# Kernel tuning notes

Measured on AMD Instinct MI355X. Metric: run time of the kernel, lower is better.

## Reference

```python
import jax, jax.numpy as jnp
import numpy as np

D_MODEL = 1024
ED = 2048          # d_inner = 2 * d_model
N = 16             # d_state
DT_RANK = 64
K = 4              # d_conv
BETA = 0.6
ALPHA = 1.0
B_SZ, L = 1, 2048


def setup_inputs() -> dict:
    key = jax.random.key(0)
    ks = jax.random.split(key, 9)
    s = 0.02
    x = jax.random.normal(ks[0], (B_SZ, L, D_MODEL), jnp.float32)
    W_in = jax.random.normal(ks[1], (2 * ED, D_MODEL), jnp.float32) * s
    conv_w = jax.random.normal(ks[2], (ED, K), jnp.float32) * s
    conv_b = jax.random.normal(ks[3], (ED,), jnp.float32) * s
    W_x = jax.random.normal(ks[4], (DT_RANK + 2 * N, ED), jnp.float32) * s
    dt_std = DT_RANK ** -0.5
    W_dt = jax.random.uniform(ks[5], (ED, DT_RANK), jnp.float32, -dt_std, dt_std)
    # dt bias init: inverse-softplus of dt in [dt_min, dt_max]
    dt = jnp.exp(jax.random.uniform(ks[6], (ED,), jnp.float32)
                 * (np.log(0.1) - np.log(0.001)) + np.log(0.001))
    dt = jnp.clip(dt, 1e-4)
    b_dt = dt + jnp.log(-jnp.expm1(-dt))
    A_log = jnp.log(jnp.tile(jnp.arange(1, N + 1, dtype=jnp.float32), (ED, 1)))
    D = jnp.ones((ED,), jnp.float32)
    W_out = jax.random.normal(ks[7], (D_MODEL, ED), jnp.float32) * s
    return {"x": x, "W_in": W_in, "conv_w": conv_w, "conv_b": conv_b,
            "W_x": W_x, "W_dt": W_dt, "b_dt": b_dt, "A_log": A_log,
            "D": D, "W_out": W_out}


def _depthwise_causal_conv(xc, conv_w, conv_b):
    # xc: (B, L, ED); torch Conv1d(groups=ED, padding=K-1)[..., :L] == causal conv
    lhs = jnp.transpose(xc, (0, 2, 1))                       # (B, ED, L)
    lhs = jnp.pad(lhs, ((0, 0), (0, 0), (K - 1, 0)))
    out = jax.lax.conv_general_dilated(lhs, conv_w[:, None, :], (1,), 'VALID',
                                       feature_group_count=ED)  # (B, ED, L)
    return jnp.transpose(out, (0, 2, 1)) + conv_b


def _ssm_momentum(xc, W_x, W_dt, b_dt, A_log, D):
    A = -jnp.exp(A_log)                                      # (ED, N)
    dBC = xc @ W_x.T                                         # (B, L, dt_rank + 2N)
    delta, Bm, Cm = jnp.split(dBC, [DT_RANK, DT_RANK + N], axis=-1)
    delta = jax.nn.softplus(delta @ W_dt.T + b_dt)           # (B, L, ED)
    deltaA = jnp.exp(delta[..., None] * A)                   # (B, L, ED, N)
    u = ALPHA * delta[..., None] * Bm[:, :, None, :] * xc[..., None]  # (B, L, ED, N)

    def step(carry, inp):
        h, v = carry
        dA_t, u_t = inp
        v = BETA * v + u_t
        h = dA_t * h + v
        return (h, v), h

    h0 = jnp.zeros((xc.shape[0], ED, N), xc.dtype)
    _, hs = jax.lax.scan(step, (h0, h0),
                         (jnp.moveaxis(deltaA, 1, 0), jnp.moveaxis(u, 1, 0)))
    y = jnp.einsum('lben,bln->ble', hs, Cm)                  # (B, L, ED)
    return y + D * xc


def reference(x, W_in, conv_w, conv_b, W_x, W_dt, b_dt, A_log, D, W_out):
    xz = x @ W_in.T                                          # (B, L, 2*ED)
    xc, z = jnp.split(xz, 2, axis=-1)
    xc = jax.nn.silu(_depthwise_causal_conv(xc, conv_w, conv_b))
    y = _ssm_momentum(xc, W_x, W_dt, b_dt, A_log, D)
    return (y * jax.nn.silu(z)) @ W_out.T                    # (B, L, d_model)
```

## Files before the change

kernel.cpp:

```cpp
#include <hip/hip_runtime.h>
#include <hip/hip_bf16.h>
#include <math.h>

#define L 2048
#define DM 1024
#define ED 2048
#define NST 16
#define DTR 64
#define BETA 0.6f
#define NCHUNK 64
#define LCH 32
#define SPLITS 16
#define SPLIT4 4

typedef __bf16 bf16_t;
typedef __bf16 bf16x8 __attribute__((ext_vector_type(8)));
typedef __bf16 bf16x4 __attribute__((ext_vector_type(4)));
typedef float  floatx4 __attribute__((ext_vector_type(4)));


__global__ void k_fill(float* __restrict__ p, float v, int n) {
    int i = blockIdx.x * 256 + threadIdx.x;
    if (i < n) p[i] = v;
}

__global__ void k_cvt_all(const float4* __restrict__ s0, bf16x4* __restrict__ d0,
                          const float4* __restrict__ s1, bf16x4* __restrict__ d1,
                          const float4* __restrict__ s2, bf16x4* __restrict__ d2,
                          const float4* __restrict__ s3, bf16x4* __restrict__ d3,
                          const float4* __restrict__ s4, bf16x4* __restrict__ d4) {
    int i = blockIdx.x * 256 + threadIdx.x;
    const float4* s; bf16x4* d; int j;
    if (i < 524288)        { s = s0; d = d0; j = i; }
    else if (i < 1572864)  { s = s1; d = d1; j = i - 524288; }
    else if (i < 1622016)  { s = s2; d = d2; j = i - 1572864; }
    else if (i < 1654784)  { s = s3; d = d3; j = i - 1622016; }
    else                   { s = s4; d = d4; j = i - 1654784; }
    float4 f = s[j];
    bf16x4 o;
    o[0] = (bf16_t)f.x; o[1] = (bf16_t)f.y; o[2] = (bf16_t)f.z; o[3] = (bf16_t)f.w;
    d[j] = o;
}

template<int EPI, bool GUARD>
__global__ __launch_bounds__(256)
void k_gemm_bt(const bf16_t* __restrict__ X, const bf16_t* __restrict__ W,
               float* __restrict__ C, int M, int N, int K, int ldc, int ksz,
               const float* __restrict__ bias) {
    __shared__ bf16_t As[128 * 32];
    __shared__ bf16_t Bs[128 * 32];
    const int tid  = threadIdx.x;
    const int bx   = blockIdx.x, by = blockIdx.y;
    const int kbase = blockIdx.z * ksz;
    const size_t zoff = (size_t)blockIdx.z * M * ldc;
    const int wave = tid >> 6, lane = tid & 63;
    const int wm   = (wave >> 1) * 64;
    const int wn   = (wave & 1) * 64;
    const int quad = lane >> 4, l16 = lane & 15;

    floatx4 acc[4][4];
#pragma unroll
    for (int i = 0; i < 4; i++)
#pragma unroll
        for (int j = 0; j < 4; j++)
            acc[i][j] = (floatx4){0.f, 0.f, 0.f, 0.f};

    for (int kt = kbase; kt < kbase + ksz; kt += 32) {
        if (GUARD) {
#pragma unroll
            for (int p = 0; p < 2; p++) {
                int e = p * 2048 + tid * 8;
                int r = e >> 5, c = e & 31;
                int arow = by * 128 + r;
                *(float4*)(&As[r * 32 + c]) =
                    *(const float4*)(&X[(size_t)arow * K + kt + c]);
                int brow = bx * 128 + r;
                float4 bv = make_float4(0.f, 0.f, 0.f, 0.f);
                if (brow < N) bv = *(const float4*)(&W[(size_t)brow * K + kt + c]);
                *(float4*)(&Bs[r * 32 + c]) = bv;
            }
        } else {
#pragma unroll
            for (int p = 0; p < 2; p++) {
                int e = p * 2048 + tid * 8;
                int r = e >> 5, c = e & 31;
                __builtin_amdgcn_global_load_lds(
                    (const __attribute__((address_space(1))) void*)&X[(size_t)(by * 128 + r) * K + kt + c],
                    (__attribute__((address_space(3))) void*)&As[e], 16, 0, 0);
                __builtin_amdgcn_global_load_lds(
                    (const __attribute__((address_space(1))) void*)&W[(size_t)(bx * 128 + r) * K + kt + c],
                    (__attribute__((address_space(3))) void*)&Bs[e], 16, 0, 0);
            }
        }
        __syncthreads();

        bf16x8 af[4], bfr[4];
#pragma unroll
        for (int mt = 0; mt < 4; mt++)
            af[mt] = *(const bf16x8*)(&As[(wm + mt * 16 + l16) * 32 + quad * 8]);
#pragma unroll
        for (int nt = 0; nt < 4; nt++)
            bfr[nt] = *(const bf16x8*)(&Bs[(wn + nt * 16 + l16) * 32 + quad * 8]);
#pragma unroll
        for (int mt = 0; mt < 4; mt++)
#pragma unroll
            for (int nt = 0; nt < 4; nt++)
                acc[mt][nt] = __builtin_amdgcn_mfma_f32_16x16x32_bf16(
                    af[mt], bfr[nt], acc[mt][nt], 0, 0, 0);
        __syncthreads();
    }

#pragma unroll
    for (int mt = 0; mt < 4; mt++) {
#pragma unroll
        for (int nt = 0; nt < 4; nt++) {
            int col = bx * 128 + wn + nt * 16 + l16;
            if (!GUARD || col < N) {
#pragma unroll
                for (int r4 = 0; r4 < 4; r4++) {
                    int row = by * 128 + wm + mt * 16 + quad * 4 + r4;
                    float v = acc[mt][nt][r4];
                    size_t off = zoff + (size_t)row * ldc + col;
                    if (EPI == 0) {
                        C[off] = v;
                    } else if (EPI == 1) {
                        v += bias[col];
                        v = (v > 20.f) ? v : __logf(1.f + __expf(v));
                        ((bf16_t*)C)[off] = (bf16_t)v;
                    } else {
                        ((bf16_t*)C)[off] = (bf16_t)v;
                    }
                }
            }
        }
    }
}

__global__ void k_red4(const bf16x8* __restrict__ part, float4* __restrict__ out) {
    int i = blockIdx.x * 256 + threadIdx.x;
    const int stride = L * DM / 8;
    bf16x8 a = part[i], b = part[i + stride];
    bf16x8 c = part[i + 2 * stride], d = part[i + 3 * stride];
    float4 o0, o1;
    o0.x = (float)a[0] + (float)b[0] + (float)c[0] + (float)d[0];
    o0.y = (float)a[1] + (float)b[1] + (float)c[1] + (float)d[1];
    o0.z = (float)a[2] + (float)b[2] + (float)c[2] + (float)d[2];
    o0.w = (float)a[3] + (float)b[3] + (float)c[3] + (float)d[3];
    o1.x = (float)a[4] + (float)b[4] + (float)c[4] + (float)d[4];
    o1.y = (float)a[5] + (float)b[5] + (float)c[5] + (float)d[5];
    o1.z = (float)a[6] + (float)b[6] + (float)c[6] + (float)d[6];
    o1.w = (float)a[7] + (float)b[7] + (float)c[7] + (float)d[7];
    out[2 * i]     = o0;
    out[2 * i + 1] = o1;
}

__global__ void k_conv_silu(const bf16_t* __restrict__ xz,
                            const float* __restrict__ conv_w,
                            const float* __restrict__ conv_b,
                            bf16_t* __restrict__ xc_bf) {
    int idx = blockIdx.x * 256 + threadIdx.x;
    int e = idx & (ED - 1);
    int t = idx >> 11;
    float w0 = conv_w[e * 4 + 0], w1 = conv_w[e * 4 + 1];
    float w2 = conv_w[e * 4 + 2], w3 = conv_w[e * 4 + 3];
    const bf16_t* col = xz + e;
    float acc = conv_b[e];
    if (t >= 3) acc += w0 * (float)col[(size_t)(t - 3) * 4096];
    if (t >= 2) acc += w1 * (float)col[(size_t)(t - 2) * 4096];
    if (t >= 1) acc += w2 * (float)col[(size_t)(t - 1) * 4096];
    acc += w3 * (float)col[(size_t)t * 4096];
    float s = acc / (1.f + __expf(-acc));
    xc_bf[idx] = (bf16_t)s;
}

__global__ void k_red2(const float* __restrict__ part, float* __restrict__ dBC,
                       bf16_t* __restrict__ dly) {
    int idx = blockIdx.x * 256 + threadIdx.x;
    int t = idx / 96, c = idx - t * 96;
    float s = 0.f;
#pragma unroll
    for (int sp = 0; sp < SPLITS; sp++) s += part[(size_t)sp * L * 96 + idx];
    dBC[idx] = s;
    if (c < 64) dly[t * 64 + c] = (bf16_t)s;
}


__global__ __launch_bounds__(256)
void k_scan_p1(const bf16_t* __restrict__ delta, const bf16_t* __restrict__ xc,
               const float* __restrict__ dBC, const float* __restrict__ A_log,
               float4* __restrict__ summ) {
    const int chunk = blockIdx.x >> 3;
    const int e = (blockIdx.x & 7) * 256 + threadIdx.x;
    float A[NST];
#pragma unroll
    for (int n = 0; n < NST; n++) A[n] = -__expf(A_log[e * NST + n]);
    float h[NST], v[NST], p[NST], q[NST];
#pragma unroll
    for (int n = 0; n < NST; n++) { h[n] = 0.f; v[n] = 0.f; p[n] = 1.f; q[n] = 0.f; }
    float bp = 1.f;
    const int t0 = chunk * LCH;
    for (int i = 0; i < LCH; i++) {
        int t = t0 + i;
        float d   = (float)delta[(size_t)t * ED + e];
        float xcv = (float)xc[(size_t)t * ED + e];
        float du  = d * xcv;
        bp *= BETA;
        const float* Bp = &dBC[t * 96 + 64];
#pragma unroll
        for (int n = 0; n < NST; n++) {
            float a = __expf(d * A[n]);
            v[n] = BETA * v[n] + du * Bp[n];
            h[n] = a * h[n] + v[n];
            p[n] *= a;
            q[n] = a * q[n] + bp;
        }
    }
#pragma unroll
    for (int n = 0; n < NST; n++)
        summ[((size_t)n * NCHUNK + chunk) * ED + e] = make_float4(h[n], v[n], p[n], q[n]);
}

__global__ void k_combine(const float4* __restrict__ summ, float2* __restrict__ inc) {
    int tid = blockIdx.x * 256 + threadIdx.x;
    int n = tid >> 11, e = tid & (ED - 1);
    float h = 0.f, v = 0.f;
    const float bl = 7.9586611e-8f;
#pragma unroll 4
    for (int c = 0; c < NCHUNK; c++) {
        size_t idx = ((size_t)n * NCHUNK + c) * ED + e;
        float4 f = summ[idx];
        inc[idx] = make_float2(h, v);
        float hn = f.z * h + f.w * v + f.x;
        v = bl * v + f.y;
        h = hn;
    }
}

__global__ __launch_bounds__(256)
void k_scan_p2(const bf16_t* __restrict__ delta, const bf16_t* __restrict__ xc,
               const float* __restrict__ dBC, const float* __restrict__ A_log,
               const float2* __restrict__ inc, const float* __restrict__ Dvec,
               const bf16_t* __restrict__ xz, bf16_t* __restrict__ g) {
    const int chunk = blockIdx.x >> 3;
    const int e = (blockIdx.x & 7) * 256 + threadIdx.x;
    float A[NST];
#pragma unroll
    for (int n = 0; n < NST; n++) A[n] = -__expf(A_log[e * NST + n]);
    float h[NST], v[NST];
#pragma unroll
    for (int n = 0; n < NST; n++) {
        float2 s = inc[((size_t)n * NCHUNK + chunk) * ED + e];
        h[n] = s.x; v[n] = s.y;
    }
    const float De = Dvec[e];
    const int t0 = chunk * LCH;
    for (int i = 0; i < LCH; i++) {
        int t = t0 + i;
        float d   = (float)delta[(size_t)t * ED + e];
        float xcv = (float)xc[(size_t)t * ED + e];
        float du  = d * xcv;
        const float* Bp = &dBC[t * 96 + 64];
        const float* Cp = &dBC[t * 96 + 80];
        float yacc = 0.f;
#pragma unroll
        for (int n = 0; n < NST; n++) {
            float a = __expf(d * A[n]);
            v[n] = BETA * v[n] + du * Bp[n];
            h[n] = a * h[n] + v[n];
            yacc += Cp[n] * h[n];
        }
        float z = (float)xz[(size_t)t * 4096 + ED + e];
        float sz = z / (1.f + __expf(-z));
        g[(size_t)t * ED + e] = (bf16_t)((yacc + De * xcv) * sz);
    }
}


extern "C" void kernel_launch(void* const* d_in, const int* in_sizes, int n_in,
                              void* d_out, int out_size, void* d_ws, size_t ws_size,
                              hipStream_t stream) {
    const float* x      = (const float*)d_in[0];
    const float* W_in   = (const float*)d_in[1];
    const float* conv_w = (const float*)d_in[2];
    const float* conv_b = (const float*)d_in[3];
    const float* W_x    = (const float*)d_in[4];
    const float* W_dt   = (const float*)d_in[5];
    const float* b_dt   = (const float*)d_in[6];
    const float* A_log  = (const float*)d_in[7];
    const float* Dv     = (const float*)d_in[8];
    const float* W_out  = (const float*)d_in[9];
    float* out = (float*)d_out;

    constexpr size_t OFF_XZ    = 0;
    constexpr size_t OFF_XC    = 33554432;
    constexpr size_t OFF_C     = 50331648;
    constexpr size_t OFF_DELTA = 58720256;
    constexpr size_t OFF_R1    = 75497472;
    constexpr size_t OFF_XBF   = 109051904;
    constexpr size_t OFF_DBC   = 113246208;
    constexpr size_t OFF_DLY   = 114032640;
    constexpr size_t OFF_WX    = 114294784;
    constexpr size_t OFF_WDT   = 114688000;
    constexpr size_t OFF_WOUT  = 114950144;
    constexpr size_t WS_NEED   = 119144448;

    if (ws_size < WS_NEED) {
        k_fill<<<(out_size + 255) / 256, 256, 0, stream>>>(out, 1.0e9f, out_size);
        return;
    }

    char* ws = (char*)d_ws;
    bf16_t* xz_bf = (bf16_t*)(ws + OFF_XZ);
    bf16_t* part4 = (bf16_t*)(ws + OFF_XZ);
    float2* inc   = (float2*)(ws + OFF_XC);
    bf16_t* xc_bf = (bf16_t*)(ws + OFF_C);
    bf16_t* delta_bf = (bf16_t*)(ws + OFF_DELTA);
    bf16_t* g_bf  = (bf16_t*)(ws + OFF_DELTA + 8388608);
    bf16_t* Win_bf  = (bf16_t*)(ws + OFF_R1);
    float*  part2   = (float*)(ws + OFF_R1 + 16777216);
    float4* summ    = (float4*)(ws + OFF_R1);
    bf16_t* x_bf  = (bf16_t*)(ws + OFF_XBF);
    float*  dBC   = (float*)(ws + OFF_DBC);
    bf16_t* dly   = (bf16_t*)(ws + OFF_DLY);
    bf16_t* Wx_bf  = (bf16_t*)(ws + OFF_WX);
    bf16_t* Wdt_bf = (bf16_t*)(ws + OFF_WDT);
    bf16_t* Wout_bf = (bf16_t*)(ws + OFF_WOUT);

    k_cvt_all<<<8512, 256, 0, stream>>>(
        (const float4*)x,     (bf16x4*)x_bf,
        (const float4*)W_in,  (bf16x4*)Win_bf,
        (const float4*)W_x,   (bf16x4*)Wx_bf,
        (const float4*)W_dt,  (bf16x4*)Wdt_bf,
        (const float4*)W_out, (bf16x4*)Wout_bf);

    {
        dim3 g(4096 / 128, L / 128, 1);
        k_gemm_bt<2, false><<<g, 256, 0, stream>>>(x_bf, Win_bf, (float*)xz_bf, L, 4096, DM, 4096, DM, nullptr);
    }
    k_conv_silu<<<L * ED / 256, 256, 0, stream>>>(xz_bf, conv_w, conv_b, xc_bf);
    {
        dim3 g(1, L / 128, SPLITS);
        k_gemm_bt<0, true><<<g, 256, 0, stream>>>(xc_bf, Wx_bf, part2, L, 96, ED, 96, ED / SPLITS, nullptr);
    }
    k_red2<<<L * 96 / 256, 256, 0, stream>>>(part2, dBC, dly);
    {
        dim3 g(ED / 128, L / 128, 1);
        k_gemm_bt<1, false><<<g, 256, 0, stream>>>(dly, Wdt_bf, (float*)delta_bf, L, ED, DTR, ED, DTR, b_dt);
    }
    k_scan_p1<<<NCHUNK * 8, 256, 0, stream>>>(delta_bf, xc_bf, dBC, A_log, summ);
    k_combine<<<ED * NST / 256, 256, 0, stream>>>(summ, inc);
    k_scan_p2<<<NCHUNK * 8, 256, 0, stream>>>(delta_bf, xc_bf, dBC, A_log, inc, Dv, xz_bf, g_bf);
    {
        dim3 g(DM / 128, L / 128, SPLIT4);
        k_gemm_bt<2, false><<<g, 256, 0, stream>>>(g_bf, Wout_bf, (float*)part4, L, DM, ED, DM, ED / SPLIT4, nullptr);
    }
    k_red4<<<L * DM / 8 / 256, 256, 0, stream>>>((const bf16x8*)part4, (float4*)out);
}
```

Before: 245.0 us.

## Fuse x conversion into in_proj GEMM, vectorize conv, compress scan summaries

The separate conversion of x to bf16 is removed, and the in_proj GEMM now reads fp32 x and converts it to bf16 while staging tiles into LDS. The depthwise conv+SiLU kernel now handles 8 channels per thread with 16-byte vector loads and stores. The scan chunk summaries are split into fp32 (h,v) and bf16 (p,q) arrays, and the combine step updates (h,v) in place, which cuts summary traffic. The risks are precision loss from storing p/q in bf16 and the synchronous A-tile loads in the GEMM, which no longer use the async global-to-LDS path.

```diff
diff --git a/kernel.cpp b/kernel.cpp
--- a/kernel.cpp
+++ b/kernel.cpp
@@ -16,6 +16,7 @@
 typedef __bf16 bf16_t;
 typedef __bf16 bf16x8 __attribute__((ext_vector_type(8)));
 typedef __bf16 bf16x4 __attribute__((ext_vector_type(4)));
+typedef __bf16 bf16x2 __attribute__((ext_vector_type(2)));
 typedef float  floatx4 __attribute__((ext_vector_type(4)));
 
 
@@ -24,29 +25,27 @@
     if (i < n) p[i] = v;
 }
 
-__global__ void k_cvt_all(const float4* __restrict__ s0, bf16x4* __restrict__ d0,
-                          const float4* __restrict__ s1, bf16x4* __restrict__ d1,
+__global__ void k_cvt_all(const float4* __restrict__ s1, bf16x4* __restrict__ d1,
                           const float4* __restrict__ s2, bf16x4* __restrict__ d2,
                           const float4* __restrict__ s3, bf16x4* __restrict__ d3,
                           const float4* __restrict__ s4, bf16x4* __restrict__ d4) {
     int i = blockIdx.x * 256 + threadIdx.x;
     const float4* s; bf16x4* d; int j;
-    if (i < 524288)        { s = s0; d = d0; j = i; }
-    else if (i < 1572864)  { s = s1; d = d1; j = i - 524288; }
-    else if (i < 1622016)  { s = s2; d = d2; j = i - 1572864; }
-    else if (i < 1654784)  { s = s3; d = d3; j = i - 1622016; }
-    else                   { s = s4; d = d4; j = i - 1654784; }
+    if (i < 1048576)       { s = s1; d = d1; j = i; }
+    else if (i < 1097728)  { s = s2; d = d2; j = i - 1048576; }
+    else if (i < 1130496)  { s = s3; d = d3; j = i - 1097728; }
+    else                   { s = s4; d = d4; j = i - 1130496; }
     float4 f = s[j];
     bf16x4 o;
     o[0] = (bf16_t)f.x; o[1] = (bf16_t)f.y; o[2] = (bf16_t)f.z; o[3] = (bf16_t)f.w;
     d[j] = o;
 }
 
-template<int EPI, bool GUARD>
+template<int EPI, bool GUARD, bool CVTA>
 __global__ __launch_bounds__(256)
 void k_gemm_bt(const bf16_t* __restrict__ X, const bf16_t* __restrict__ W,
                float* __restrict__ C, int M, int N, int K, int ldc, int ksz,
-               const float* __restrict__ bias) {
+               const float* __restrict__ bias, const float* __restrict__ Xf) {
     __shared__ bf16_t As[128 * 32];
     __shared__ bf16_t Bs[128 * 32];
     const int tid  = threadIdx.x;
@@ -78,6 +77,29 @@
                 float4 bv = make_float4(0.f, 0.f, 0.f, 0.f);
                 if (brow < N) bv = *(const float4*)(&W[(size_t)brow * K + kt + c]);
                 *(float4*)(&Bs[r * 32 + c]) = bv;
+            }
+        } else if (CVTA) {
+#pragma unroll
+            for (int p = 0; p < 2; p++) {
+                int e = p * 2048 + tid * 8;
+                int r = e >> 5, c = e & 31;
+                __builtin_amdgcn_global_load_lds(
+                    (const __attribute__((address_space(1))) void*)&W[(size_t)(bx * 128 + r) * K + kt + c],
+                    (__attribute__((address_space(3))) void*)&Bs[e], 16, 0, 0);
+            }
+#pragma unroll
+            for (int p = 0; p < 2; p++) {
+                int e = p * 2048 + tid * 8;
+                int r = e >> 5, c = e & 31;
+                const float* src = &Xf[(size_t)(by * 128 + r) * K + kt + c];
+                float4 f0 = *(const float4*)src;
+                float4 f1 = *(const float4*)(src + 4);
+                bf16x8 o;
+                o[0] = (bf16_t)f0.x; o[1] = (bf16_t)f0.y;
+                o[2] = (bf16_t)f0.z; o[3] = (bf16_t)f0.w;
+                o[4] = (bf16_t)f1.x; o[5] = (bf16_t)f1.y;
+                o[6] = (bf16_t)f1.z; o[7] = (bf16_t)f1.w;
+                *(bf16x8*)(&As[e]) = o;
             }
         } else {
 #pragma unroll
@@ -159,18 +181,33 @@
                             const float* __restrict__ conv_b,
                             bf16_t* __restrict__ xc_bf) {
     int idx = blockIdx.x * 256 + threadIdx.x;
-    int e = idx & (ED - 1);
-    int t = idx >> 11;
-    float w0 = conv_w[e * 4 + 0], w1 = conv_w[e * 4 + 1];
-    float w2 = conv_w[e * 4 + 2], w3 = conv_w[e * 4 + 3];
-    const bf16_t* col = xz + e;
-    float acc = conv_b[e];
-    if (t >= 3) acc += w0 * (float)col[(size_t)(t - 3) * 4096];
-    if (t >= 2) acc += w1 * (float)col[(size_t)(t - 2) * 4096];
-    if (t >= 1) acc += w2 * (float)col[(size_t)(t - 1) * 4096];
-    acc += w3 * (float)col[(size_t)t * 4096];
-    float s = acc / (1.f + __expf(-acc));
-    xc_bf[idx] = (bf16_t)s;
+    int t  = idx >> 8;
+    int e8 = (idx & 255) * 8;
+    float4 w[8];
+#pragma unroll
+    for (int j = 0; j < 8; j++) w[j] = *(const float4*)(&conv_w[(e8 + j) * 4]);
+    float acc[8];
+#pragma unroll
+    for (int j = 0; j < 8; j++) acc[j] = conv_b[e8 + j];
+#pragma unroll
+    for (int k = 0; k < 4; k++) {
+        int tt = t - (3 - k);
+        if (tt >= 0) {
+            bf16x8 v = *(const bf16x8*)(xz + (size_t)tt * 4096 + e8);
+            const float* wk = (const float*)w;
+#pragma unroll
+            for (int j = 0; j < 8; j++)
+                acc[j] += ((const float*)&w[j])[k] * (float)v[j];
+            (void)wk;
+        }
+    }
+    bf16x8 o;
+#pragma unroll
+    for (int j = 0; j < 8; j++) {
+        float s = acc[j] / (1.f + __expf(-acc[j]));
+        o[j] = (bf16_t)s;
+    }
+    *(bf16x8*)(xc_bf + (size_t)t * ED + e8) = o;
 }
 
 __global__ void k_red2(const float* __restrict__ part, float* __restrict__ dBC,
@@ -188,7 +225,7 @@
 __global__ __launch_bounds__(256)
 void k_scan_p1(const bf16_t* __restrict__ delta, const bf16_t* __restrict__ xc,
                const float* __restrict__ dBC, const float* __restrict__ A_log,
-               float4* __restrict__ summ) {
+               float2* __restrict__ hv, bf16x2* __restrict__ pq) {
     const int chunk = blockIdx.x >> 3;
     const int e = (blockIdx.x & 7) * 256 + threadIdx.x;
     float A[NST];
@@ -216,11 +253,15 @@
         }
     }
 #pragma unroll
-    for (int n = 0; n < NST; n++)
-        summ[((size_t)n * NCHUNK + chunk) * ED + e] = make_float4(h[n], v[n], p[n], q[n]);
-}
-
-__global__ void k_combine(const float4* __restrict__ summ, float2* __restrict__ inc) {
+    for (int n = 0; n < NST; n++) {
+        size_t idx = ((size_t)n * NCHUNK + chunk) * ED + e;
+        hv[idx] = make_float2(h[n], v[n]);
+        bf16x2 z; z[0] = (bf16_t)p[n]; z[1] = (bf16_t)q[n];
+        pq[idx] = z;
+    }
+}
+
+__global__ void k_combine(float2* __restrict__ hv, const bf16x2* __restrict__ pq) {
     int tid = blockIdx.x * 256 + threadIdx.x;
     int n = tid >> 11, e = tid & (ED - 1);
     float h = 0.f, v = 0.f;
@@ -228,9 +269,10 @@
 #pragma unroll 4
     for (int c = 0; c < NCHUNK; c++) {
         size_t idx = ((size_t)n * NCHUNK + c) * ED + e;
-        float4 f = summ[idx];
-        inc[idx] = make_float2(h, v);
-        float hn = f.z * h + f.w * v + f.x;
+        float2 f = hv[idx];
+        bf16x2 z = pq[idx];
+        hv[idx] = make_float2(h, v);
+        float hn = (float)z[0] * h + (float)z[1] * v + f.x;
         v = bl * v + f.y;
         h = hn;
     }
@@ -239,7 +281,7 @@
 __global__ __launch_bounds__(256)
 void k_scan_p2(const bf16_t* __restrict__ delta, const bf16_t* __restrict__ xc,
                const float* __restrict__ dBC, const float* __restrict__ A_log,
-               const float2* __restrict__ inc, const float* __restrict__ Dvec,
+               const float2* __restrict__ hv, const float* __restrict__ Dvec,
                const bf16_t* __restrict__ xz, bf16_t* __restrict__ g) {
     const int chunk = blockIdx.x >> 3;
     const int e = (blockIdx.x & 7) * 256 + threadIdx.x;
@@ -249,7 +291,7 @@
     float h[NST], v[NST];
 #pragma unroll
     for (int n = 0; n < NST; n++) {
-        float2 s = inc[((size_t)n * NCHUNK + chunk) * ED + e];
+        float2 s = hv[((size_t)n * NCHUNK + chunk) * ED + e];
         h[n] = s.x; v[n] = s.y;
     }
     const float De = Dvec[e];
@@ -312,22 +354,20 @@
     char* ws = (char*)d_ws;
     bf16_t* xz_bf = (bf16_t*)(ws + OFF_XZ);
     bf16_t* part4 = (bf16_t*)(ws + OFF_XZ);
-    float2* inc   = (float2*)(ws + OFF_XC);
+    float2* hv    = (float2*)(ws + OFF_XC);
     bf16_t* xc_bf = (bf16_t*)(ws + OFF_C);
     bf16_t* delta_bf = (bf16_t*)(ws + OFF_DELTA);
     bf16_t* g_bf  = (bf16_t*)(ws + OFF_DELTA + 8388608);
     bf16_t* Win_bf  = (bf16_t*)(ws + OFF_R1);
     float*  part2   = (float*)(ws + OFF_R1 + 16777216);
-    float4* summ    = (float4*)(ws + OFF_R1);
-    bf16_t* x_bf  = (bf16_t*)(ws + OFF_XBF);
+    bf16x2* pq      = (bf16x2*)(ws + OFF_R1);
     float*  dBC   = (float*)(ws + OFF_DBC);
     bf16_t* dly   = (bf16_t*)(ws + OFF_DLY);
     bf16_t* Wx_bf  = (bf16_t*)(ws + OFF_WX);
     bf16_t* Wdt_bf = (bf16_t*)(ws + OFF_WDT);
     bf16_t* Wout_bf = (bf16_t*)(ws + OFF_WOUT);
 
-    k_cvt_all<<<8512, 256, 0, stream>>>(
-        (const float4*)x,     (bf16x4*)x_bf,
+    k_cvt_all<<<6464, 256, 0, stream>>>(
         (const float4*)W_in,  (bf16x4*)Win_bf,
         (const float4*)W_x,   (bf16x4*)Wx_bf,
         (const float4*)W_dt,  (bf16x4*)Wdt_bf,
@@ -335,24 +375,28 @@
 
     {
         dim3 g(4096 / 128, L / 128, 1);
-        k_gemm_bt<2, false><<<g, 256, 0, stream>>>(x_bf, Win_bf, (float*)xz_bf, L, 4096, DM, 4096, DM, nullptr);
-    }
-    k_conv_silu<<<L * ED / 256, 256, 0, stream>>>(xz_bf, conv_w, conv_b, xc_bf);
+        k_gemm_bt<2, false, true><<<g, 256, 0, stream>>>(
+            nullptr, Win_bf, (float*)xz_bf, L, 4096, DM, 4096, DM, nullptr, x);
+    }
+    k_conv_silu<<<L * ED / 8 / 256, 256, 0, stream>>>(xz_bf, conv_w, conv_b, xc_bf);
     {
         dim3 g(1, L / 128, SPLITS);
-        k_gemm_bt<0, true><<<g, 256, 0, stream>>>(xc_bf, Wx_bf, part2, L, 96, ED, 96, ED / SPLITS, nullptr);
+        k_gemm_bt<0, true, false><<<g, 256, 0, stream>>>(
+            xc_bf, Wx_bf, part2, L, 96, ED, 96, ED / SPLITS, nullptr, nullptr);
     }
     k_red2<<<L * 96 / 256, 256, 0, stream>>>(part2, dBC, dly);
     {
         dim3 g(ED / 128, L / 128, 1);
-        k_gemm_bt<1, false><<<g, 256, 0, stream>>>(dly, Wdt_bf, (float*)delta_bf, L, ED, DTR, ED, DTR, b_dt);
-    }
-    k_scan_p1<<<NCHUNK * 8, 256, 0, stream>>>(delta_bf, xc_bf, dBC, A_log, summ);
-    k_combine<<<ED * NST / 256, 256, 0, stream>>>(summ, inc);
-    k_scan_p2<<<NCHUNK * 8, 256, 0, stream>>>(delta_bf, xc_bf, dBC, A_log, inc, Dv, xz_bf, g_bf);
+        k_gemm_bt<1, false, false><<<g, 256, 0, stream>>>(
+            dly, Wdt_bf, (float*)delta_bf, L, ED, DTR, ED, DTR, b_dt, nullptr);
+    }
+    k_scan_p1<<<NCHUNK * 8, 256, 0, stream>>>(delta_bf, xc_bf, dBC, A_log, hv, pq);
+    k_combine<<<ED * NST / 256, 256, 0, stream>>>(hv, pq);
+    k_scan_p2<<<NCHUNK * 8, 256, 0, stream>>>(delta_bf, xc_bf, dBC, A_log, hv, Dv, xz_bf, g_bf);
     {
         dim3 g(DM / 128, L / 128, SPLIT4);
-        k_gemm_bt<2, false><<<g, 256, 0, stream>>>(g_bf, Wout_bf, (float*)part4, L, DM, ED, DM, ED / SPLIT4, nullptr);
+        k_gemm_bt<2, false, false><<<g, 256, 0, stream>>>(
+            g_bf, Wout_bf, (float*)part4, L, DM, ED, DM, ED / SPLIT4, nullptr, nullptr);
     }
     k_red4<<<L * DM / 8 / 256, 256, 0, stream>>>((const bf16x8*)part4, (float4*)out);
 }
```

Measured after the change: 258.1 us. +5.3%, slower.
